# Kernel optimization log

Measured on AMD Instinct MI355X. Metric: run time of the kernel, lower is better.

The kernel has to match this reference:

```python
import jax, jax.numpy as jnp
import numpy as np

SMOOTHNESS_RATIO = 0.2
DEGREE_RATIO = 0.1
SPARSITY_RATIO = 0.1
VERY_SMALL_NUMBER = 1e-12


def setup_inputs() -> dict:
    key = jax.random.key(0)
    k1, k2 = jax.random.split(key)
    B, N, D = 64, 1024, 16
    out_adj = jax.random.uniform(k1, (B, N, N), dtype=jnp.float32)  # nonneg adjacency (softmax-like)
    features = jax.random.normal(k2, (B, N, D), dtype=jnp.float32)
    return {"out_adj": out_adj, "features": features}


def reference(out_adj, features):
    # Faithful fused version of add_batch_graph_loss with keep_batch_dim=True.
    # Per sample i: smoothness_ratio * tr(F^T (diag(deg) - A) F) / (N*N)
    #   tr(F^T diag(deg) F) = sum_n deg_n ||f_n||^2
    #   tr(F^T A F)        = sum(F * (A @ F))
    B, N, _ = out_adj.shape
    denom = jnp.float32(N * N)

    deg = jnp.sum(out_adj, axis=-1)                       # [B, N] row degrees
    AF = jnp.einsum('bij,bjd->bid', out_adj, features)    # [B, N, D]
    smooth = (jnp.einsum('bn,bnd->b', deg, features * features)
              - jnp.einsum('bnd,bnd->b', features, AF))   # [B] = tr(F^T L F)
    graph_loss = SMOOTHNESS_RATIO * smooth / denom

    # degree regularization: -degree_ratio * ones^T log(A @ ones + eps) / N
    # A @ ones == deg
    log_degrees = jnp.log(deg + VERY_SMALL_NUMBER)        # [B, N]
    graph_loss = graph_loss - DEGREE_RATIO * jnp.sum(log_degrees, axis=-1) / N

    # sparsity: sparsity_ratio * sum(A^2) / (N*N)
    graph_loss = graph_loss + SPARSITY_RATIO * jnp.sum(out_adj * out_adj, axis=(1, 2)) / denom
    return graph_loss  # [B]
```

## Files before the change

kernel.cpp:

```cpp
#include <hip/hip_runtime.h>


#define NN      1024
#define DD      16
#define ROWS    64
#define TPB     256
#define CH      16
#define SMOOTHR 0.2f
#define DEGRR   0.1f
#define SPARSR  0.1f
#define EPSV    1e-12f

__global__ __launch_bounds__(TPB, 4)
void graph_loss_kernel(const float* __restrict__ A,
                       const float* __restrict__ F,
                       float* __restrict__ out) {
    __shared__ float fn_lds[ROWS][DD];
    __shared__ float fn2_lds[ROWS];
    __shared__ float degpart[TPB][CH + 1];
    __shared__ float wred[4][3];

    const int tid = threadIdx.x;
    const int bid = blockIdx.x;
    const int b   = bid >> 4;
    const int n0  = (bid & 15) * ROWS;

    const float* __restrict__ Fb = F + (size_t)b * NN * DD;
    const float* __restrict__ Ab = A + ((size_t)b * NN + n0) * NN;

    {
        const int r = tid >> 2, q = tid & 3;
        const float4 v = *(const float4*)(Fb + (size_t)(n0 + r) * DD + q * 4);
        *(float4*)&fn_lds[r][q * 4] = v;
    }

    float fj[4][DD];
    #pragma unroll
    for (int jj = 0; jj < 4; ++jj) {
        const float* p = Fb + (size_t)(4 * tid + jj) * DD;
        #pragma unroll
        for (int q = 0; q < 4; ++q) {
            const float4 v = *(const float4*)(p + 4 * q);
            fj[jj][4 * q + 0] = v.x;
            fj[jj][4 * q + 1] = v.y;
            fj[jj][4 * q + 2] = v.z;
            fj[jj][4 * q + 3] = v.w;
        }
    }
    __syncthreads();

    if (tid < ROWS) {
        float s = 0.f;
        #pragma unroll
        for (int d = 0; d < DD; ++d) s += fn_lds[tid][d] * fn_lds[tid][d];
        fn2_lds[tid] = s;
    }
    __syncthreads();

    float sm = 0.f;
    float sq = 0.f;
    float lg = 0.f;

    const float* __restrict__ arow = Ab + 4 * tid;
    float4 cur = *(const float4*)(arow);

    for (int c = 0; c < ROWS / CH; ++c) {
        for (int rr = 0; rr < CH; ++rr) {
            const int r = c * CH + rr;
            const float4 a = cur;
            if (r + 1 < ROWS)
                cur = *(const float4*)(arow + (size_t)(r + 1) * NN);

            const float av[4] = {a.x, a.y, a.z, a.w};

            degpart[tid][rr] = av[0] + av[1] + av[2] + av[3];
            sq += av[0] * av[0] + av[1] * av[1] + av[2] * av[2] + av[3] * av[3];

            float fn[DD];
            #pragma unroll
            for (int q = 0; q < 4; ++q)
                *(float4*)&fn[4 * q] = *(const float4*)&fn_lds[r][4 * q];
            const float fn2 = fn2_lds[r];

            #pragma unroll
            for (int jj = 0; jj < 4; ++jj) {
                float dt = 0.f;
                #pragma unroll
                for (int d = 0; d < DD; ++d) dt += fj[jj][d] * fn[d];
                sm += av[jj] * (fn2 - dt);
            }
        }

        __syncthreads();
        {
            const int r = tid >> 4, seg = tid & 15;
            float s = 0.f;
            #pragma unroll
            for (int i = 0; i < 16; ++i) s += degpart[seg * 16 + i][r];
            s += __shfl_xor(s, 1);
            s += __shfl_xor(s, 2);
            s += __shfl_xor(s, 4);
            s += __shfl_xor(s, 8);
            if (seg == 0) lg += logf(s + EPSV);
        }
        __syncthreads();
    }

    #pragma unroll
    for (int m = 1; m < 64; m <<= 1) {
        sm += __shfl_xor(sm, m);
        sq += __shfl_xor(sq, m);
        lg += __shfl_xor(lg, m);
    }
    const int w = tid >> 6, lane = tid & 63;
    if (lane == 0) { wred[w][0] = sm; wred[w][1] = sq; wred[w][2] = lg; }
    __syncthreads();
    if (tid == 0) {
        float S = 0.f, Q = 0.f, L = 0.f;
        #pragma unroll
        for (int i = 0; i < 4; ++i) { S += wred[i][0]; Q += wred[i][1]; L += wred[i][2]; }
        const float denom = (float)NN * (float)NN;
        const float contrib = SMOOTHR * S / denom
                            - DEGRR * L / (float)NN
                            + SPARSR * Q / denom;
        atomicAdd(out + b, contrib);
    }
}

extern "C" void kernel_launch(void* const* d_in, const int* in_sizes, int n_in,
                              void* d_out, int out_size, void* d_ws, size_t ws_size,
                              hipStream_t stream) {
    const float* A = (const float*)d_in[0];
    const float* F = (const float*)d_in[1];
    float* out = (float*)d_out;

    const int B = out_size;
    hipMemsetAsync(d_out, 0, (size_t)B * sizeof(float), stream);
    graph_loss_kernel<<<dim3(B * (NN / ROWS)), dim3(TPB), 0, stream>>>(A, F, out);
}
```

Baseline: 367.1 us.

## Deepen row prefetch and defer degree reduction to a single final pass

Replaces the single-row register prefetch with a 4-deep ring of in-flight row loads so more global memory requests are outstanding per thread. Row degrees are now partially reduced with lane shuffles and stored once per 4-lane group into an LDS table. They are summed only after the main loop, which removes the per-chunk barriers and LDS transposed reduction. The log-degree term is computed only in wave 0, so thread 0 holds the full sum. The cost is more registers for the prefetch buffer and a serial 64-element LDS sum at the end.

```diff
diff --git a/kernel.cpp b/kernel.cpp
--- a/kernel.cpp
+++ b/kernel.cpp
@@ -5,7 +5,7 @@
 #define DD      16
 #define ROWS    64
 #define TPB     256
-#define CH      16
+#define PF      4
 #define SMOOTHR 0.2f
 #define DEGRR   0.1f
 #define SPARSR  0.1f
@@ -17,8 +17,8 @@
                        float* __restrict__ out) {
     __shared__ float fn_lds[ROWS][DD];
     __shared__ float fn2_lds[ROWS];
-    __shared__ float degpart[TPB][CH + 1];
-    __shared__ float wred[4][3];
+    __shared__ float degq[ROWS][65];
+    __shared__ float wred[4][2];
 
     const int tid = threadIdx.x;
     const int bid = blockIdx.x;
@@ -28,27 +28,22 @@
     const float* __restrict__ Fb = F + (size_t)b * NN * DD;
     const float* __restrict__ Ab = A + ((size_t)b * NN + n0) * NN;
 
+    float4 fj[4][4];
+    {
+        const float* p = Fb + (size_t)(4 * tid) * DD;
+        #pragma unroll
+        for (int jj = 0; jj < 4; ++jj)
+            #pragma unroll
+            for (int q = 0; q < 4; ++q)
+                fj[jj][q] = *(const float4*)(p + jj * DD + 4 * q);
+    }
+
     {
         const int r = tid >> 2, q = tid & 3;
-        const float4 v = *(const float4*)(Fb + (size_t)(n0 + r) * DD + q * 4);
-        *(float4*)&fn_lds[r][q * 4] = v;
-    }
-
-    float fj[4][DD];
-    #pragma unroll
-    for (int jj = 0; jj < 4; ++jj) {
-        const float* p = Fb + (size_t)(4 * tid + jj) * DD;
-        #pragma unroll
-        for (int q = 0; q < 4; ++q) {
-            const float4 v = *(const float4*)(p + 4 * q);
-            fj[jj][4 * q + 0] = v.x;
-            fj[jj][4 * q + 1] = v.y;
-            fj[jj][4 * q + 2] = v.z;
-            fj[jj][4 * q + 3] = v.w;
-        }
+        *(float4*)&fn_lds[r][4 * q] =
+            *(const float4*)(Fb + (size_t)(n0 + r) * DD + 4 * q);
     }
     __syncthreads();
-
     if (tid < ROWS) {
         float s = 0.f;
         #pragma unroll
@@ -57,53 +52,59 @@
     }
     __syncthreads();
 
-    float sm = 0.f;
-    float sq = 0.f;
-    float lg = 0.f;
+    float sm = 0.f, sq = 0.f;
 
     const float* __restrict__ arow = Ab + 4 * tid;
-    float4 cur = *(const float4*)(arow);
+    const int  g       = tid >> 2;
+    const bool deglane = (tid & 3) == 0;
 
-    for (int c = 0; c < ROWS / CH; ++c) {
-        for (int rr = 0; rr < CH; ++rr) {
-            const int r = c * CH + rr;
-            const float4 a = cur;
-            if (r + 1 < ROWS)
-                cur = *(const float4*)(arow + (size_t)(r + 1) * NN);
+    auto process = [&](const float4 a, const int r) {
+        float s = (a.x + a.y) + (a.z + a.w);
+        s += __shfl_xor(s, 1);
+        s += __shfl_xor(s, 2);
+        if (deglane) degq[r][g] = s;
 
-            const float av[4] = {a.x, a.y, a.z, a.w};
+        sq += a.x * a.x + a.y * a.y + a.z * a.z + a.w * a.w;
 
-            degpart[tid][rr] = av[0] + av[1] + av[2] + av[3];
-            sq += av[0] * av[0] + av[1] * av[1] + av[2] * av[2] + av[3] * av[3];
+        float dt0 = 0.f, dt1 = 0.f, dt2 = 0.f, dt3 = 0.f;
+        #pragma unroll
+        for (int q = 0; q < 4; ++q) {
+            const float4 f = *(const float4*)&fn_lds[r][4 * q];
+            dt0 += fj[0][q].x * f.x + fj[0][q].y * f.y + fj[0][q].z * f.z + fj[0][q].w * f.w;
+            dt1 += fj[1][q].x * f.x + fj[1][q].y * f.y + fj[1][q].z * f.z + fj[1][q].w * f.w;
+            dt2 += fj[2][q].x * f.x + fj[2][q].y * f.y + fj[2][q].z * f.z + fj[2][q].w * f.w;
+            dt3 += fj[3][q].x * f.x + fj[3][q].y * f.y + fj[3][q].z * f.z + fj[3][q].w * f.w;
+        }
+        const float fn2 = fn2_lds[r];
+        sm += a.x * (fn2 - dt0) + a.y * (fn2 - dt1)
+            + a.z * (fn2 - dt2) + a.w * (fn2 - dt3);
+    };
 
-            float fn[DD];
-            #pragma unroll
-            for (int q = 0; q < 4; ++q)
-                *(float4*)&fn[4 * q] = *(const float4*)&fn_lds[r][4 * q];
-            const float fn2 = fn2_lds[r];
+    float4 buf[PF];
+    #pragma unroll
+    for (int i = 0; i < PF; ++i)
+        buf[i] = *(const float4*)(arow + (size_t)i * NN);
 
-            #pragma unroll
-            for (int jj = 0; jj < 4; ++jj) {
-                float dt = 0.f;
-                #pragma unroll
-                for (int d = 0; d < DD; ++d) dt += fj[jj][d] * fn[d];
-                sm += av[jj] * (fn2 - dt);
-            }
+    #pragma unroll 1
+    for (int rb = 0; rb < ROWS - PF; rb += PF) {
+        #pragma unroll
+        for (int k = 0; k < PF; ++k) {
+            const float4 a = buf[k];
+            buf[k] = *(const float4*)(arow + (size_t)(rb + k + PF) * NN);
+            process(a, rb + k);
         }
+    }
+    #pragma unroll
+    for (int k = 0; k < PF; ++k)
+        process(buf[k], ROWS - PF + k);
 
-        __syncthreads();
-        {
-            const int r = tid >> 4, seg = tid & 15;
-            float s = 0.f;
-            #pragma unroll
-            for (int i = 0; i < 16; ++i) s += degpart[seg * 16 + i][r];
-            s += __shfl_xor(s, 1);
-            s += __shfl_xor(s, 2);
-            s += __shfl_xor(s, 4);
-            s += __shfl_xor(s, 8);
-            if (seg == 0) lg += logf(s + EPSV);
-        }
-        __syncthreads();
+    __syncthreads();
+    float lg = 0.f;
+    if (tid < ROWS) {
+        float s = 0.f;
+        #pragma unroll 1
+        for (int i = 0; i < ROWS; ++i) s += degq[tid][i];
+        lg = logf(s + EPSV);
     }
 
     #pragma unroll
@@ -112,16 +113,16 @@
         sq += __shfl_xor(sq, m);
         lg += __shfl_xor(lg, m);
     }
-    const int w = tid >> 6, lane = tid & 63;
-    if (lane == 0) { wred[w][0] = sm; wred[w][1] = sq; wred[w][2] = lg; }
+    const int w = tid >> 6;
+    if ((tid & 63) == 0) { wred[w][0] = sm; wred[w][1] = sq; }
     __syncthreads();
     if (tid == 0) {
-        float S = 0.f, Q = 0.f, L = 0.f;
+        float S = 0.f, Q = 0.f;
         #pragma unroll
-        for (int i = 0; i < 4; ++i) { S += wred[i][0]; Q += wred[i][1]; L += wred[i][2]; }
+        for (int i = 0; i < 4; ++i) { S += wred[i][0]; Q += wred[i][1]; }
         const float denom = (float)NN * (float)NN;
         const float contrib = SMOOTHR * S / denom
-                            - DEGRR * L / (float)NN
+                            - DEGRR * lg / (float)NN
                             + SPARSR * Q / denom;
         atomicAdd(out + b, contrib);
     }
```

Result: slower. 687.1 us (+87.2%).
